# Optimization experiments

Hardware: AMD Instinct MI355X
Metric: run time of the kernel (lower is better)

The kernel has to match this reference:

```python
import jax, jax.numpy as jnp
import numpy as np

N_EMBD = 1024
N_HEAD = 16
HEAD_DIM = N_EMBD // N_HEAD

def setup_inputs() -> dict:
    key = jax.random.key(0)
    ks = jax.random.split(key, 9)
    B, T, C = 2, 2048, N_EMBD
    s = 1.0 / np.sqrt(C)
    x = jax.random.normal(ks[0], (B, T, C), dtype=jnp.float32)
    Wk = jax.random.normal(ks[1], (C, C), dtype=jnp.float32) * s
    bk = jnp.zeros((C,), dtype=jnp.float32)
    Wq = jax.random.normal(ks[2], (C, C), dtype=jnp.float32) * s
    bq = jnp.zeros((C,), dtype=jnp.float32)
    Wv = jax.random.normal(ks[3], (C, C), dtype=jnp.float32) * s
    bv = jnp.zeros((C,), dtype=jnp.float32)
    Wp = jax.random.normal(ks[4], (C, C), dtype=jnp.float32) * s
    bp = jnp.zeros((C,), dtype=jnp.float32)
    return {"x": x, "Wq": Wq, "bq": bq, "Wk": Wk, "bk": bk, "Wv": Wv, "bv": bv, "Wp": Wp, "bp": bp}

def reference(x, Wq, bq, Wk, bk, Wv, bv, Wp, bp):
    B, T, C = x.shape
    H, D = N_HEAD, HEAD_DIM
    # QKV projections (torch Linear: x @ W.T + b; here W is stored as (in,out))
    q = (x @ Wq + bq).reshape(B, T, H, D).transpose(0, 2, 1, 3)  # [B,H,T,D]
    k = (x @ Wk + bk).reshape(B, T, H, D).transpose(0, 2, 1, 3)
    v = (x @ Wv + bv).reshape(B, T, H, D).transpose(0, 2, 1, 3)
    att = jnp.einsum('bhtd,bhsd->bhts', q, k) / jnp.sqrt(jnp.float32(D))
    causal = jnp.tril(jnp.ones((T, T), dtype=bool))
    att = jnp.where(causal, att, jnp.float32(-jnp.inf))
    att = jax.nn.softmax(att, axis=-1)
    y = jnp.einsum('bhts,bhsd->bhtd', att, v)  # [B,H,T,D]
    y = y.transpose(0, 2, 1, 3).reshape(B, T, C)
    return y @ Wp + bp
```

## Files before the change

kernel.cpp:

```cpp
#include <hip/hip_runtime.h>
#include <cstdint>

typedef __attribute__((ext_vector_type(4))) short s16x4;
typedef __attribute__((ext_vector_type(8))) short s16x8;
typedef __attribute__((ext_vector_type(4))) float f32x4;
typedef __attribute__((ext_vector_type(16))) float f32x16;

#define L2E 1.44269504088896340736f

__device__ __forceinline__ short f2bf(float f) {
  union { float f; unsigned u; } v; v.f = f;
  unsigned r = (v.u + 0x7fffu + ((v.u >> 16) & 1u)) >> 16;
  return (short)r;
}

__device__ __forceinline__ float xhalf_f(float x) {
  union { float f; unsigned u; } a; a.f = x;
  auto r = __builtin_amdgcn_permlane32_swap(a.u, a.u, false, false);
  union { unsigned u; float f; } b;
  b.u = (threadIdx.x & 32) ? r[0] : r[1];
  return b.f;
}

typedef const __attribute__((address_space(1))) unsigned int* gas_p;
typedef __attribute__((address_space(3))) unsigned int* las_p;
__device__ __forceinline__ void stage16(const void* g, void* l) {
  __builtin_amdgcn_global_load_lds((gas_p)(uintptr_t)g,
                                   (las_p)(unsigned int)(uintptr_t)l, 16, 0, 0);
}

__global__ __launch_bounds__(256) void cvt_bf16(const float* __restrict__ in,
                                                short* __restrict__ out) {
  int i = blockIdx.x * 256 + threadIdx.x;
  const f32x4* p = (const f32x4*)in + (size_t)i * 2;
  f32x4 a = p[0], b = p[1];
  s16x8 o;
  o[0] = f2bf(a[0]); o[1] = f2bf(a[1]); o[2] = f2bf(a[2]); o[3] = f2bf(a[3]);
  o[4] = f2bf(b[0]); o[5] = f2bf(b[1]); o[6] = f2bf(b[2]); o[7] = f2bf(b[3]);
  *((s16x8*)out + i) = o;
}

__global__ __launch_bounds__(256) void transpose_w4(const float* __restrict__ W0,
                                                    const float* __restrict__ W1,
                                                    const float* __restrict__ W2,
                                                    const float* __restrict__ W3,
                                                    short* __restrict__ dst) {
  __shared__ float tile[64][65];
  const int z = blockIdx.z;
  const float* in = (z == 0) ? W0 : (z == 1) ? W1 : (z == 2) ? W2 : W3;
  short* out = dst + (size_t)z * 1048576;
  const int bi = blockIdx.y, bj = blockIdx.x;
  const int t = threadIdx.x;
  const int c = t & 63, r0 = t >> 6;
#pragma unroll
  for (int i = 0; i < 16; i++) {
    int r = r0 + i * 4;
    tile[r][c] = in[(size_t)(bi * 64 + r) * 1024 + bj * 64 + c];
  }
  __syncthreads();
#pragma unroll
  for (int i = 0; i < 16; i++) {
    int r = r0 + i * 4;
    out[(size_t)(bj * 64 + r) * 1024 + bi * 64 + c] = f2bf(tile[c][r]);
  }
}

template <int EPI, int BM>
__global__ __launch_bounds__(BM * 2) void gemm_bt(
    const short* __restrict__ A, const short* __restrict__ B, int N, int K,
    const float* __restrict__ b0, const float* __restrict__ b1,
    const float* __restrict__ b2, short* __restrict__ o0, short* __restrict__ o1,
    short* __restrict__ o2, float* __restrict__ ofp) {
  constexpr int T = BM * 2;
  constexpr int BROUNDS = 512 / BM;
  __shared__ short As[2][BM * 32];
  __shared__ short Bs[2][128 * 32];
  const int tid = threadIdx.x;
  const int lane = tid & 63;
  const int wave = tid >> 6;
  const int wr = wave >> 1, wc = wave & 1;
  const int l15 = lane & 15, l4 = lane >> 4;
  const int id = blockIdx.x + gridDim.x * blockIdx.y;
  const int cpx = gridDim.x >> 3;
  const int xcd = id & 7, sub = id >> 3;
  const int m0 = (sub / cpx) * BM;
  const int n0 = (xcd * cpx + sub % cpx) * 128;
  const short* Ab = A + (size_t)m0 * K;
  const short* Bb = B + (size_t)n0 * K;
  f32x4 acc[4][4];
#pragma unroll
  for (int i = 0; i < 4; i++)
#pragma unroll
    for (int j = 0; j < 4; j++) acc[i][j] = (f32x4){0.f, 0.f, 0.f, 0.f};

  const int lq = tid & 3, lr = tid >> 2;
  int soffA[4], goffA[4];
#pragma unroll
  for (int i = 0; i < 4; i++) {
    const int p = i >> 1;
    const int r = (i & 1) * (BM / 2) + lr;
    soffA[i] = p * BM * 32 + r * 32 + lq * 8;
    goffA[i] = r * K + p * 32 + lq * 8;
  }
  int soffB[BROUNDS], goffB[BROUNDS];
#pragma unroll
  for (int j = 0; j < BROUNDS; j++) {
    const int flat = j * (T / 4) + lr;
    const int p = flat >> 7, r = flat & 127;
    soffB[j] = p * 128 * 32 + r * 32 + lq * 8;
    goffB[j] = r * K + p * 32 + lq * 8;
  }

  for (int k0 = 0; k0 < K; k0 += 64) {
#pragma unroll
    for (int i = 0; i < 4; i++)
      stage16(Ab + (size_t)(goffA[i] + k0), (short*)As + soffA[i]);
#pragma unroll
    for (int j = 0; j < BROUNDS; j++)
      stage16(Bb + (size_t)(goffB[j] + k0), (short*)Bs + soffB[j]);
    __syncthreads();
#pragma unroll
    for (int ks = 0; ks < 2; ks++) {
      s16x8 af[4], bfr[4];
#pragma unroll
      for (int i = 0; i < 4; i++) {
        af[i] = *(const s16x8*)((short*)As + ks * BM * 32 + (wr * 64 + i * 16 + l15) * 32 + l4 * 8);
        bfr[i] = *(const s16x8*)((short*)Bs + ks * 4096 + (wc * 64 + i * 16 + l15) * 32 + l4 * 8);
      }
#pragma unroll
      for (int mi = 0; mi < 4; mi++)
#pragma unroll
        for (int ni = 0; ni < 4; ni++)
          acc[mi][ni] = __builtin_amdgcn_mfma_f32_16x16x32_bf16(af[mi], bfr[ni],
                                                                acc[mi][ni], 0, 0, 0);
    }
    __syncthreads();
  }

#pragma unroll
  for (int ni = 0; ni < 4; ni++) {
    const int col = n0 + wc * 64 + ni * 16 + l15;
    if (EPI == 1) {
      const float bias = b0[col];
#pragma unroll
      for (int mi = 0; mi < 4; mi++)
#pragma unroll
        for (int r = 0; r < 4; r++) {
          int row = m0 + wr * 64 + mi * 16 + l4 * 4 + r;
          ofp[(size_t)row * N + col] = acc[mi][ni][r] + bias;
        }
    } else {
      const float* bp; short* dst; int c1; int isV = 0; float scl = 1.0f;
      if (col < 1024) { bp = b0; dst = o0; c1 = col; scl = 0.125f * L2E; }
      else if (col < 2048) { bp = b1; dst = o1; c1 = col - 1024; }
      else { bp = b2; dst = o2; c1 = col - 2048; isV = 1; }
      const float bias = bp[c1];
      const int h = c1 >> 6, d = c1 & 63;
      if (isV) {
#pragma unroll
        for (int mi = 0; mi < 4; mi++) {
          int t0 = m0 + wr * 64 + mi * 16 + l4 * 4;
          int bb = t0 >> 11, t = t0 & 2047;
          s16x4 ov;
#pragma unroll
          for (int r = 0; r < 4; r++) ov[r] = f2bf(acc[mi][ni][r] + bias);
          *(s16x4*)(dst + (size_t)((bb * 16 + h) * 64 + d) * 2048 + t) = ov;
        }
      } else {
#pragma unroll
        for (int mi = 0; mi < 4; mi++)
#pragma unroll
          for (int r = 0; r < 4; r++) {
            int row = m0 + wr * 64 + mi * 16 + l4 * 4 + r;
            int bb = row >> 11, t = row & 2047;
            float v = (acc[mi][ni][r] + bias) * scl;
            dst[(size_t)((bb * 16 + h) * 2048 + t) * 64 + d] = f2bf(v);
          }
      }
    }
  }
}

__global__ __launch_bounds__(128) void attn_v7(const short* __restrict__ Q,
                                               const short* __restrict__ K,
                                               const short* __restrict__ Vt,
                                               short* __restrict__ Y) {
  __shared__ short Ks[2][64 * 64];
  __shared__ short Vs[3][64 * 64];
  const int bh = blockIdx.x;
  const int qt = 31 - (int)blockIdx.y;
  const int tid = threadIdx.x, lane = tid & 63, wave = tid >> 6;
  const int q31 = lane & 31, hi = lane >> 5;
  const short* Qp = Q + (size_t)bh * 2048 * 64;
  const short* Kp = K + (size_t)bh * 2048 * 64;
  const short* Vp = Vt + (size_t)bh * 64 * 2048;
  const int qrow = qt * 64 + wave * 32 + q31;
  const int nt = qt + 1;
  const int cx = q31 & 7;

  s16x8 qf[4];
#pragma unroll
  for (int s = 0; s < 4; s++)
    qf[s] = *(const s16x8*)(Qp + (size_t)qrow * 64 + s * 16 + hi * 8);

  f32x16 accA, accB, Z;
#pragma unroll
  for (int i = 0; i < 16; i++) { accA[i] = 0.f; accB[i] = 0.f; Z[i] = 0.f; }
  float l = 0.f;

  const int srow = tid >> 3, sch = tid & 7;
  int sdst[4], koff[4], voff[4];
#pragma unroll
  for (int i = 0; i < 4; i++) {
    const int r = srow + i * 16;
    const int sc = sch ^ (r & 7);
    sdst[i] = r * 64 + sch * 8;
    koff[i] = r * 64 + sc * 8;
    voff[i] = r * 2048 + sc * 8;
  }
  const short* kst = Kp;
  const short* vst = Vp;
  int rd0[4];
#pragma unroll
  for (int s = 0; s < 4; s++) rd0[s] = q31 * 64 + (((2 * s + hi) ^ cx) << 3);

  short* kA = &Ks[0][0]; short* kB = &Ks[1][0];
  short* vP = &Vs[2][0]; short* vC = &Vs[0][0]; short* vN = &Vs[1][0];

#pragma unroll
  for (int i = 0; i < 4; i++) {
    stage16(kst + koff[i], kA + sdst[i]);
    stage16(vst + voff[i], vC + sdst[i]);
  }
  kst += 4096; vst += 64;

#define STAGE_NEXT(COND)                                                       \
  if (COND) {                                                                  \
    _Pragma("unroll") for (int i_ = 0; i_ < 4; i_++) {                         \
      stage16(kst + koff[i_], kB + sdst[i_]);                                  \
      stage16(vst + voff[i_], vN + sdst[i_]);                                  \
    }                                                                          \
    kst += 4096; vst += 64;                                                    \
  }

#define QK(S0, S1)                                                             \
  {                                                                            \
    s16x8 kf0_[4], kf1_[4];                                                    \
    _Pragma("unroll") for (int s_ = 0; s_ < 4; s_++) {                         \
      kf0_[s_] = *(const s16x8*)(kA + rd0[s_]);                                \
      kf1_[s_] = *(const s16x8*)(kA + rd0[s_] + 2048);                         \
    }                                                                          \
    __builtin_amdgcn_s_setprio(1);                                             \
    S0 = __builtin_amdgcn_mfma_f32_32x32x16_bf16(kf0_[0], qf[0], Z, 0, 0, 0);  \
    S1 = __builtin_amdgcn_mfma_f32_32x32x16_bf16(kf1_[0], qf[0], Z, 0, 0, 0);  \
    _Pragma("unroll") for (int s_ = 1; s_ < 4; s_++) {                         \
      S0 = __builtin_amdgcn_mfma_f32_32x32x16_bf16(kf0_[s_], qf[s_], S0, 0, 0, 0); \
      S1 = __builtin_amdgcn_mfma_f32_32x32x16_bf16(kf1_[s_], qf[s_], S1, 0, 0, 0); \
    }                                                                          \
    __builtin_amdgcn_s_setprio(0);                                             \
  }

#define SMPV_BODY(S0, S1)                                                      \
  {                                                                            \
    float rsum_ = 0.f;                                                         \
    _Pragma("unroll") for (int r_ = 0; r_ < 16; r_++) {                        \
      float p_ = __builtin_amdgcn_exp2f(S0[r_]);                               \
      S0[r_] = p_; rsum_ += p_;                                                \
    }                                                                          \
    _Pragma("unroll") for (int r_ = 0; r_ < 16; r_++) {                        \
      float p_ = __builtin_amdgcn_exp2f(S1[r_]);                               \
      S1[r_] = p_; rsum_ += p_;                                                \
    }                                                                          \
    l += rsum_;                                                                \
    unsigned pk0_[8], pk1_[8];                                                 \
    _Pragma("unroll") for (int j_ = 0; j_ < 8; j_++) {                         \
      unsigned u_;                                                             \
      float a0_ = S0[2 * j_], a1_ = S0[2 * j_ + 1];                            \
      asm("v_cvt_pk_bf16_f32 %0, %1, %2" : "=v"(u_) : "v"(a0_), "v"(a1_));     \
      pk0_[j_] = u_;                                                           \
      float b0_ = S1[2 * j_], b1_ = S1[2 * j_ + 1];                            \
      asm("v_cvt_pk_bf16_f32 %0, %1, %2" : "=v"(u_) : "v"(b0_), "v"(b1_));     \
      pk1_[j_] = u_;                                                           \
    }                                                                          \
    _Pragma("unroll") for (int s_ = 0; s_ < 4; s_++) {                         \
      const unsigned* pk_ = (s_ < 2) ? pk0_ : pk1_;                            \
      const int b_ = 4 * (s_ & 1);                                             \
      auto rA_ = __builtin_amdgcn_permlane32_swap(pk_[b_ + 0], pk_[b_ + 2], false, false); \
      auto rB_ = __builtin_amdgcn_permlane32_swap(pk_[b_ + 1], pk_[b_ + 3], false, false); \
      union { unsigned u[4]; s16x8 v; } fr_;                                   \
      fr_.u[0] = rA_[0]; fr_.u[1] = rB_[0]; fr_.u[2] = rA_[1]; fr_.u[3] = rB_[1]; \
      s16x8 vf0_ = *(const s16x8*)(vP + rd0[s_]);                              \
      s16x8 vf1_ = *(const s16x8*)(vP + rd0[s_] + 2048);                       \
      __builtin_amdgcn_s_setprio(1);                                           \
      accA = __builtin_amdgcn_mfma_f32_32x32x16_bf16(vf0_, fr_.v, accA, 0, 0, 0); \
      accB = __builtin_amdgcn_mfma_f32_32x32x16_bf16(vf1_, fr_.v, accB, 0, 0, 0); \
      __builtin_amdgcn_s_setprio(0);                                           \
    }                                                                          \
  }

#define SMPV_MASK(S0, S1)                                                      \
  {                                                                            \
    const int k0_ = (nt - 1) * 64;                                             \
    _Pragma("unroll") for (int r_ = 0; r_ < 16; r_++) {                        \
      int kvr_ = k0_ + (r_ & 3) + 8 * (r_ >> 2) + 4 * hi;                      \
      if (kvr_ > qrow) S0[r_] = -__builtin_inff();                             \
      if (kvr_ + 32 > qrow) S1[r_] = -__builtin_inff();                        \
    }                                                                          \
    SMPV_BODY(S0, S1)                                                          \
  }

#define ROT()                                                                  \
  {                                                                            \
    short* t_ = kA; kA = kB; kB = t_;                                          \
    t_ = vP; vP = vC; vC = vN; vN = t_;                                        \
  }

  f32x16 sA0, sA1, sB0, sB1;
  __syncthreads();
  STAGE_NEXT(nt > 1)
  QK(sA0, sA1)
  ROT()
  int t = 1;
  for (; t + 1 < nt; t += 2) {
    __syncthreads();
    STAGE_NEXT(t + 1 < nt)
    QK(sB0, sB1)
    SMPV_BODY(sA0, sA1)
    ROT()
    __syncthreads();
    STAGE_NEXT(t + 2 < nt)
    QK(sA0, sA1)
    SMPV_BODY(sB0, sB1)
    ROT()
  }
  if (t < nt) {
    __syncthreads();
    QK(sB0, sB1)
    SMPV_BODY(sA0, sA1)
    ROT()
    SMPV_MASK(sB0, sB1)
  } else {
    SMPV_MASK(sA0, sA1)
  }
#undef STAGE_NEXT
#undef QK
#undef SMPV_BODY
#undef SMPV_MASK
#undef ROT

  const int b_ = bh >> 4, h_ = bh & 15;
  const float lt = l + xhalf_f(l);
  const float invl = 1.f / lt;
  const size_t base = ((size_t)b_ * 2048 + qrow) * 1024 + h_ * 64;
#pragma unroll
  for (int g = 0; g < 4; g++) {
    s16x4 o0, o1;
#pragma unroll
    for (int e = 0; e < 4; e++) {
      o0[e] = f2bf(accA[4 * g + e] * invl);
      o1[e] = f2bf(accB[4 * g + e] * invl);
    }
    *(s16x4*)(Y + base + 8 * g + 4 * hi) = o0;
    *(s16x4*)(Y + base + 32 + 8 * g + 4 * hi) = o1;
  }
}

extern "C" void kernel_launch(void* const* d_in, const int* in_sizes, int n_in,
                              void* d_out, int out_size, void* d_ws, size_t ws_size,
                              hipStream_t stream) {
  const float* x = (const float*)d_in[0];
  const float* Wq = (const float*)d_in[1];
  const float* bq = (const float*)d_in[2];
  const float* Wk = (const float*)d_in[3];
  const float* bk = (const float*)d_in[4];
  const float* Wv = (const float*)d_in[5];
  const float* bv = (const float*)d_in[6];
  const float* Wp = (const float*)d_in[7];
  const float* bp = (const float*)d_in[8];
  float* out = (float*)d_out;
  char* ws = (char*)d_ws;

  short* xb    = (short*)(ws + 0);
  short* WqkvT = (short*)(ws + 8388608);
  short* WpT   = (short*)(ws + 14680064);
  short* Qb    = (short*)(ws + 16777216);
  short* Kb    = (short*)(ws + 25165824);
  short* Vtb   = (short*)(ws + 33554432);
  short* Yb    = xb;

  cvt_bf16<<<2048, 256, 0, stream>>>(x, xb);
  transpose_w4<<<dim3(16, 16, 4), 256, 0, stream>>>(Wq, Wk, Wv, Wp, WqkvT);
  gemm_bt<0, 256><<<dim3(24, 16), 512, 0, stream>>>(xb, WqkvT, 3072, 1024, bq, bk, bv,
                                                    Qb, Kb, Vtb, nullptr);
  attn_v7<<<dim3(32, 32), 128, 0, stream>>>(Qb, Kb, Vtb, Yb);
  gemm_bt<1, 128><<<dim3(8, 32), 256, 0, stream>>>(Yb, WpT, 1024, 1024, bp, nullptr,
                                                   nullptr, nullptr, nullptr, nullptr, out);
}
```

Baseline: 117.0 us.

## Fuse prepass kernels, retile output projection, and reorder attention query tiles

The x conversion and the weight transpose now run in one combined prepass launch, which saves a kernel launch. The GEMM template gains a BN parameter so the output projection can use 64x128 tiles with 128 threads and twice as many blocks, for better CU occupancy. The attention kernel replaces its simple reverse query-tile order with a serpentine order rotated by head, to balance causal work across the concurrently running blocks. Risks: the smaller projection tiles reuse less data per block, and the new attention order may schedule the heavy tiles last.

```diff
diff --git a/kernel.cpp b/kernel.cpp
--- a/kernel.cpp
+++ b/kernel.cpp
@@ -29,28 +29,29 @@
                                    (las_p)(unsigned int)(uintptr_t)l, 16, 0, 0);
 }
 
-__global__ __launch_bounds__(256) void cvt_bf16(const float* __restrict__ in,
-                                                short* __restrict__ out) {
-  int i = blockIdx.x * 256 + threadIdx.x;
-  const f32x4* p = (const f32x4*)in + (size_t)i * 2;
-  f32x4 a = p[0], b = p[1];
-  s16x8 o;
-  o[0] = f2bf(a[0]); o[1] = f2bf(a[1]); o[2] = f2bf(a[2]); o[3] = f2bf(a[3]);
-  o[4] = f2bf(b[0]); o[5] = f2bf(b[1]); o[6] = f2bf(b[2]); o[7] = f2bf(b[3]);
-  *((s16x8*)out + i) = o;
-}
-
-__global__ __launch_bounds__(256) void transpose_w4(const float* __restrict__ W0,
-                                                    const float* __restrict__ W1,
-                                                    const float* __restrict__ W2,
-                                                    const float* __restrict__ W3,
-                                                    short* __restrict__ dst) {
+__global__ __launch_bounds__(256) void prepass(const float* __restrict__ W0,
+                                               const float* __restrict__ W1,
+                                               const float* __restrict__ W2,
+                                               const float* __restrict__ W3,
+                                               short* __restrict__ wdst,
+                                               const float* __restrict__ x,
+                                               short* __restrict__ xb) {
+  const int z = blockIdx.z;
+  const int t = threadIdx.x;
+  if (z >= 4) {
+    int i = ((z - 4) * 256 + blockIdx.y * 16 + blockIdx.x) * 256 + t;
+    const f32x4* p = (const f32x4*)x + (size_t)i * 2;
+    f32x4 a = p[0], b = p[1];
+    s16x8 o;
+    o[0] = f2bf(a[0]); o[1] = f2bf(a[1]); o[2] = f2bf(a[2]); o[3] = f2bf(a[3]);
+    o[4] = f2bf(b[0]); o[5] = f2bf(b[1]); o[6] = f2bf(b[2]); o[7] = f2bf(b[3]);
+    *((s16x8*)xb + i) = o;
+    return;
+  }
   __shared__ float tile[64][65];
-  const int z = blockIdx.z;
   const float* in = (z == 0) ? W0 : (z == 1) ? W1 : (z == 2) ? W2 : W3;
-  short* out = dst + (size_t)z * 1048576;
+  short* out = wdst + (size_t)z * 1048576;
   const int bi = blockIdx.y, bj = blockIdx.x;
-  const int t = threadIdx.x;
   const int c = t & 63, r0 = t >> 6;
 #pragma unroll
   for (int i = 0; i < 16; i++) {
@@ -65,26 +66,27 @@
   }
 }
 
-template <int EPI, int BM>
-__global__ __launch_bounds__(BM * 2) void gemm_bt(
+template <int EPI, int BM, int BN>
+__global__ __launch_bounds__((BM / 64) * (BN / 64) * 64) void gemm_bt(
     const short* __restrict__ A, const short* __restrict__ B, int N, int K,
     const float* __restrict__ b0, const float* __restrict__ b1,
     const float* __restrict__ b2, short* __restrict__ o0, short* __restrict__ o1,
     short* __restrict__ o2, float* __restrict__ ofp) {
-  constexpr int T = BM * 2;
-  constexpr int BROUNDS = 512 / BM;
+  constexpr int T = (BM / 64) * (BN / 64) * 64;
+  constexpr int AR = BM * 8 / T;
+  constexpr int BR = BN * 8 / T;
   __shared__ short As[2][BM * 32];
-  __shared__ short Bs[2][128 * 32];
+  __shared__ short Bs[2][BN * 32];
   const int tid = threadIdx.x;
   const int lane = tid & 63;
   const int wave = tid >> 6;
-  const int wr = wave >> 1, wc = wave & 1;
+  const int wr = wave / (BN / 64), wc = wave % (BN / 64);
   const int l15 = lane & 15, l4 = lane >> 4;
   const int id = blockIdx.x + gridDim.x * blockIdx.y;
   const int cpx = gridDim.x >> 3;
   const int xcd = id & 7, sub = id >> 3;
   const int m0 = (sub / cpx) * BM;
-  const int n0 = (xcd * cpx + sub % cpx) * 128;
+  const int n0 = (xcd * cpx + sub % cpx) * BN;
   const short* Ab = A + (size_t)m0 * K;
   const short* Bb = B + (size_t)n0 * K;
   f32x4 acc[4][4];
@@ -94,29 +96,29 @@
     for (int j = 0; j < 4; j++) acc[i][j] = (f32x4){0.f, 0.f, 0.f, 0.f};
 
   const int lq = tid & 3, lr = tid >> 2;
-  int soffA[4], goffA[4];
-#pragma unroll
-  for (int i = 0; i < 4; i++) {
-    const int p = i >> 1;
-    const int r = (i & 1) * (BM / 2) + lr;
+  int soffA[AR], goffA[AR];
+#pragma unroll
+  for (int i = 0; i < AR; i++) {
+    const int flat = i * (T / 4) + lr;
+    const int p = flat / BM, r = flat % BM;
     soffA[i] = p * BM * 32 + r * 32 + lq * 8;
     goffA[i] = r * K + p * 32 + lq * 8;
   }
-  int soffB[BROUNDS], goffB[BROUNDS];
-#pragma unroll
-  for (int j = 0; j < BROUNDS; j++) {
+  int soffB[BR], goffB[BR];
+#pragma unroll
+  for (int j = 0; j < BR; j++) {
     const int flat = j * (T / 4) + lr;
-    const int p = flat >> 7, r = flat & 127;
-    soffB[j] = p * 128 * 32 + r * 32 + lq * 8;
+    const int p = flat / BN, r = flat % BN;
+    soffB[j] = p * BN * 32 + r * 32 + lq * 8;
     goffB[j] = r * K + p * 32 + lq * 8;
   }
 
   for (int k0 = 0; k0 < K; k0 += 64) {
 #pragma unroll
-    for (int i = 0; i < 4; i++)
+    for (int i = 0; i < AR; i++)
       stage16(Ab + (size_t)(goffA[i] + k0), (short*)As + soffA[i]);
 #pragma unroll
-    for (int j = 0; j < BROUNDS; j++)
+    for (int j = 0; j < BR; j++)
       stage16(Bb + (size_t)(goffB[j] + k0), (short*)Bs + soffB[j]);
     __syncthreads();
 #pragma unroll
@@ -125,7 +127,7 @@
 #pragma unroll
       for (int i = 0; i < 4; i++) {
         af[i] = *(const s16x8*)((short*)As + ks * BM * 32 + (wr * 64 + i * 16 + l15) * 32 + l4 * 8);
-        bfr[i] = *(const s16x8*)((short*)Bs + ks * 4096 + (wc * 64 + i * 16 + l15) * 32 + l4 * 8);
+        bfr[i] = *(const s16x8*)((short*)Bs + ks * BN * 32 + (wc * 64 + i * 16 + l15) * 32 + l4 * 8);
       }
 #pragma unroll
       for (int mi = 0; mi < 4; mi++)
@@ -181,14 +183,17 @@
   }
 }
 
-__global__ __launch_bounds__(128) void attn_v7(const short* __restrict__ Q,
+__global__ __launch_bounds__(128) void attn_v8(const short* __restrict__ Q,
                                                const short* __restrict__ K,
                                                const short* __restrict__ Vt,
                                                short* __restrict__ Y) {
   __shared__ short Ks[2][64 * 64];
   __shared__ short Vs[3][64 * 64];
   const int bh = blockIdx.x;
-  const int qt = 31 - (int)blockIdx.y;
+  const int y = blockIdx.y;
+  const int g = y >> 3, r_ = y & 7;
+  const int qbase = (g << 3) | ((g & 1) ? (7 - r_) : r_);
+  const int qt = (qbase + ((bh & 3) << 3)) & 31;
   const int tid = threadIdx.x, lane = tid & 63, wave = tid >> 6;
   const int q31 = lane & 31, hi = lane >> 5;
   const short* Qp = Q + (size_t)bh * 2048 * 64;
@@ -263,13 +268,13 @@
 #define SMPV_BODY(S0, S1)                                                      \
   {                                                                            \
     float rsum_ = 0.f;                                                         \
-    _Pragma("unroll") for (int r_ = 0; r_ < 16; r_++) {                        \
-      float p_ = __builtin_amdgcn_exp2f(S0[r_]);                               \
-      S0[r_] = p_; rsum_ += p_;                                                \
-    }                                                                          \
-    _Pragma("unroll") for (int r_ = 0; r_ < 16; r_++) {                        \
-      float p_ = __builtin_amdgcn_exp2f(S1[r_]);                               \
-      S1[r_] = p_; rsum_ += p_;                                                \
+    _Pragma("unroll") for (int r2_ = 0; r2_ < 16; r2_++) {                     \
+      float p_ = __builtin_amdgcn_exp2f(S0[r2_]);                              \
+      S0[r2_] = p_; rsum_ += p_;                                               \
+    }                                                                          \
+    _Pragma("unroll") for (int r2_ = 0; r2_ < 16; r2_++) {                     \
+      float p_ = __builtin_amdgcn_exp2f(S1[r2_]);                              \
+      S1[r2_] = p_; rsum_ += p_;                                               \
     }                                                                          \
     l += rsum_;                                                                \
     unsigned pk0_[8], pk1_[8];                                                 \
@@ -301,10 +306,10 @@
 #define SMPV_MASK(S0, S1)                                                      \
   {                                                                            \
     const int k0_ = (nt - 1) * 64;                                             \
-    _Pragma("unroll") for (int r_ = 0; r_ < 16; r_++) {                        \
-      int kvr_ = k0_ + (r_ & 3) + 8 * (r_ >> 2) + 4 * hi;                      \
-      if (kvr_ > qrow) S0[r_] = -__builtin_inff();                             \
-      if (kvr_ + 32 > qrow) S1[r_] = -__builtin_inff();                        \
+    _Pragma("unroll") for (int r2_ = 0; r2_ < 16; r2_++) {                     \
+      int kvr_ = k0_ + (r2_ & 3) + 8 * (r2_ >> 2) + 4 * hi;                    \
+      if (kvr_ > qrow) S0[r2_] = -__builtin_inff();                            \
+      if (kvr_ + 32 > qrow) S1[r2_] = -__builtin_inff();                       \
     }                                                                          \
     SMPV_BODY(S0, S1)                                                          \
   }
@@ -353,15 +358,15 @@
   const float invl = 1.f / lt;
   const size_t base = ((size_t)b_ * 2048 + qrow) * 1024 + h_ * 64;
 #pragma unroll
-  for (int g = 0; g < 4; g++) {
+  for (int gg = 0; gg < 4; gg++) {
     s16x4 o0, o1;
 #pragma unroll
     for (int e = 0; e < 4; e++) {
-      o0[e] = f2bf(accA[4 * g + e] * invl);
-      o1[e] = f2bf(accB[4 * g + e] * invl);
+      o0[e] = f2bf(accA[4 * gg + e] * invl);
+      o1[e] = f2bf(accB[4 * gg + e] * invl);
     }
-    *(s16x4*)(Y + base + 8 * g + 4 * hi) = o0;
-    *(s16x4*)(Y + base + 32 + 8 * g + 4 * hi) = o1;
+    *(s16x4*)(Y + base + 8 * gg + 4 * hi) = o0;
+    *(s16x4*)(Y + base + 32 + 8 * gg + 4 * hi) = o1;
   }
 }
 
@@ -388,11 +393,12 @@
   short* Vtb   = (short*)(ws + 33554432);
   short* Yb    = xb;
 
-  cvt_bf16<<<2048, 256, 0, stream>>>(x, xb);
-  transpose_w4<<<dim3(16, 16, 4), 256, 0, stream>>>(Wq, Wk, Wv, Wp, WqkvT);
-  gemm_bt<0, 256><<<dim3(24, 16), 512, 0, stream>>>(xb, WqkvT, 3072, 1024, bq, bk, bv,
-                                                    Qb, Kb, Vtb, nullptr);
-  attn_v7<<<dim3(32, 32), 128, 0, stream>>>(Qb, Kb, Vtb, Yb);
-  gemm_bt<1, 128><<<dim3(8, 32), 256, 0, stream>>>(Yb, WpT, 1024, 1024, bp, nullptr,
-                                                   nullptr, nullptr, nullptr, nullptr, out);
-}
+  prepass<<<dim3(16, 16, 12), 256, 0, stream>>>(Wq, Wk, Wv, Wp, WqkvT, x, xb);
+  gemm_bt<0, 256, 128><<<dim3(24, 16), 512, 0, stream>>>(xb, WqkvT, 3072, 1024,
+                                                         bq, bk, bv, Qb, Kb, Vtb,
+                                                         nullptr);
+  attn_v8<<<dim3(32, 32), 128, 0, stream>>>(Qb, Kb, Vtb, Yb);
+  gemm_bt<1, 64, 128><<<dim3(8, 64), 128, 0, stream>>>(Yb, WpT, 1024, 1024, bp,
+                                                       nullptr, nullptr, nullptr,
+                                                       nullptr, nullptr, out);
+}
```

New measurement: 108.3 us. -7.5%, faster.
